# Kernel tuning notes

Measured on AMD Instinct MI355X. Metric: run time of the kernel, lower is better.

Reference implementation:

```python
import jax, jax.numpy as jnp
import numpy as np

TOPK = 10
STEP = 0.1

def setup_inputs() -> dict:
    key = jax.random.key(0)
    k1, k2 = jax.random.split(key)
    input = jax.random.normal(k1, (65536, 2048), dtype=jnp.float32)
    target = jax.random.normal(k2, (65536,), dtype=jnp.float32)
    return {"input": input, "target": target}

def reference(input, target):
    # topk over last dim: values [N,k], indices [N,k]
    values, indices = jax.lax.top_k(input, TOPK)
    # diag(value @ (index*step+1).T) == row-wise dot product
    weights = indices.astype(values.dtype) * STEP + 1.0
    pred = jnp.sum(values * weights, axis=-1)  # [N]
    return jnp.mean(jnp.square(target - pred))
```

## Files before the change

kernel.cpp:

```cpp
#include <hip/hip_runtime.h>

#define COLS 2048
#define TOPK 10

typedef float f32x4 __attribute__((ext_vector_type(4)));

__global__ __launch_bounds__(256, 4) void topk_mse_main(
    const float* __restrict__ input,
    const float* __restrict__ target,
    float* __restrict__ partials)
{
    const int lane = threadIdx.x & 63;
    const int wv   = threadIdx.x >> 6;
    const int row  = (blockIdx.x << 2) + wv;

    const f32x4* rp4 = reinterpret_cast<const f32x4*>(input + (size_t)row * COLS) + lane;
    const float tgt = target[row];

    float e[32];
#pragma unroll
    for (int j = 0; j < 8; ++j) {
        f32x4 v = __builtin_nontemporal_load(rp4 + j * 64);
        e[4*j+0] = v.x; e[4*j+1] = v.y; e[4*j+2] = v.z; e[4*j+3] = v.w;
    }

    float m16[16];
#pragma unroll
    for (int i = 0; i < 16; ++i) m16[i] = fmaxf(e[2*i], e[2*i+1]);
#pragma unroll
    for (int i = 0; i < 8; ++i)  m16[i] = fmaxf(m16[2*i], m16[2*i+1]);
#pragma unroll
    for (int i = 0; i < 4; ++i)  m16[i] = fmaxf(m16[2*i], m16[2*i+1]);
    float m0 = fmaxf(fmaxf(m16[0], m16[1]), fmaxf(m16[2], m16[3]));

    float s = m0;
#pragma unroll
    for (int k = 2; k <= 64; k <<= 1) {
        const bool bk = (lane & k) != 0;
#pragma unroll
        for (int j = k >> 1; j > 0; j >>= 1) {
            float p = __shfl_xor(s, j);
            const bool take_min = (((lane & j) != 0) == bk);
            s = take_min ? fminf(s, p) : fmaxf(s, p);
        }
    }
    const float t0 = __shfl(s, 64 - TOPK);

    const float A = 1.0f + 0.4f * (float)lane;
    float s0 = 0.0f, s1 = 0.0f, s2 = 0.0f, s3 = 0.0f;
    int cnt = 0;
#pragma unroll
    for (int i = 0; i < 32; ++i) {
        const bool c = (e[i] >= t0);
        cnt += __popcll(__ballot(c));
        const float m = c ? e[i] : 0.0f;
        const float offw = 0.1f * (float)(((i >> 2) << 8) + (i & 3));
        if ((i & 3) == 0)      { s0 = fmaf(m, A, fmaf(m, offw, s0)); }
        else if ((i & 3) == 1) { s1 = fmaf(m, A, fmaf(m, offw, s1)); }
        else if ((i & 3) == 2) { s2 = fmaf(m, A, fmaf(m, offw, s2)); }
        else                   { s3 = fmaf(m, A, fmaf(m, offw, s3)); }
    }
    float sum = (s0 + s1) + (s2 + s3);
#pragma unroll
    for (int off = 32; off >= 1; off >>= 1)
        sum += __shfl_xor(sum, off);

    int excess = cnt - TOPK;
    unsigned removed = 0;
    while (excess > 0) {
        float lv = __builtin_inff();
        int   lc = -1;
#pragma unroll
        for (int i = 0; i < 32; ++i) {
            const int col = (lane << 2) + ((i >> 2) << 8) + (i & 3);
            const bool act = (e[i] >= t0) && !((removed >> i) & 1u);
            const bool better = act && ((e[i] < lv) || (e[i] == lv && col > lc));
            lv = better ? e[i] : lv;
            lc = better ? col  : lc;
        }
#pragma unroll
        for (int off = 32; off >= 1; off >>= 1) {
            const float pv = __shfl_xor(lv, off);
            const int   pc = __shfl_xor(lc, off);
            const bool take = (pv < lv) || (pv == lv && pc > lc);
            lv = take ? pv : lv;
            lc = take ? pc : lc;
        }
        sum -= lv * ((float)lc * 0.1f + 1.0f);
        if (((lc >> 2) & 63) == lane) {
            const int i = ((lc >> 8) << 2) | (lc & 3);
            removed |= (1u << i);
        }
        --excess;
    }

    __shared__ float ps[4];
    if (lane == 0) {
        const float d = tgt - sum;
        ps[wv] = d * d;
    }
    __syncthreads();
    if (threadIdx.x == 0)
        partials[blockIdx.x] = (ps[0] + ps[1]) + (ps[2] + ps[3]);
}

__global__ __launch_bounds__(256) void topk_mse_reduce(
    const float* __restrict__ partials,
    float* __restrict__ out,
    int nb, float inv_n)
{
    const f32x4* p4 = reinterpret_cast<const f32x4*>(partials);
    const int nv = nb >> 2;
    double s = 0.0;
    for (int i = threadIdx.x; i < nv; i += 256) {
        f32x4 v = p4[i];
        s += (double)v.x + (double)v.y + (double)v.z + (double)v.w;
    }
#pragma unroll
    for (int off = 32; off >= 1; off >>= 1) s += __shfl_xor(s, off);
    __shared__ double ws[4];
    const int wv = threadIdx.x >> 6;
    if ((threadIdx.x & 63) == 0) ws[wv] = s;
    __syncthreads();
    if (threadIdx.x == 0)
        out[0] = (float)(((ws[0] + ws[1]) + (ws[2] + ws[3])) * (double)inv_n);
}

extern "C" void kernel_launch(void* const* d_in, const int* in_sizes, int n_in,
                              void* d_out, int out_size, void* d_ws, size_t ws_size,
                              hipStream_t stream) {
    const float* input  = (const float*)d_in[0];
    const float* target = (const float*)d_in[1];
    float* out = (float*)d_out;
    float* partials = (float*)d_ws;

    const int rows = in_sizes[1];
    const int nb = rows / 4;
    const float inv_n = 1.0f / (float)rows;

    topk_mse_main<<<nb, 256, 0, stream>>>(input, target, partials);
    topk_mse_reduce<<<1, 256, 0, stream>>>(partials, out, nb, inv_n);
}
```

Baseline: 90.83 us.

## Make waves persistent over 16 rows with double-buffered register row prefetch

The kernel now launches a fixed 4096 waves (1024 blocks), each processing 16 rows strided by 4096. The next row is loaded into a second register buffer while the current row's top-10 selection and weighted sum run, so memory latency overlaps with compute. Each wave accumulates its squared errors in double and writes one partial, which removes the per-block shared-memory reduction and shrinks the partials array. The cost is doubled register use per thread (64 floats of row data), which can lower occupancy, and the row count is hardcoded to 65536.

```diff
diff --git a/kernel.cpp b/kernel.cpp
--- a/kernel.cpp
+++ b/kernel.cpp
@@ -2,28 +2,23 @@
 
 #define COLS 2048
 #define TOPK 10
+#define NWAVES 4096
+#define RPW 16
 
 typedef float f32x4 __attribute__((ext_vector_type(4)));
 
-__global__ __launch_bounds__(256, 4) void topk_mse_main(
-    const float* __restrict__ input,
-    const float* __restrict__ target,
-    float* __restrict__ partials)
-{
-    const int lane = threadIdx.x & 63;
-    const int wv   = threadIdx.x >> 6;
-    const int row  = (blockIdx.x << 2) + wv;
-
+__device__ __forceinline__ void load_row(const float* __restrict__ input,
+                                         int row, int lane, float (&e)[32]) {
     const f32x4* rp4 = reinterpret_cast<const f32x4*>(input + (size_t)row * COLS) + lane;
-    const float tgt = target[row];
-
-    float e[32];
 #pragma unroll
     for (int j = 0; j < 8; ++j) {
         f32x4 v = __builtin_nontemporal_load(rp4 + j * 64);
         e[4*j+0] = v.x; e[4*j+1] = v.y; e[4*j+2] = v.z; e[4*j+3] = v.w;
     }
+}
 
+__device__ __forceinline__ float row_weighted_top10(const float (&e)[32],
+                                                    int lane, float A) {
     float m16[16];
 #pragma unroll
     for (int i = 0; i < 16; ++i) m16[i] = fmaxf(e[2*i], e[2*i+1]);
@@ -46,8 +41,7 @@
     }
     const float t0 = __shfl(s, 64 - TOPK);
 
-    const float A = 1.0f + 0.4f * (float)lane;
-    float s0 = 0.0f, s1 = 0.0f, s2 = 0.0f, s3 = 0.0f;
+    float s0 = 0.f, s1 = 0.f, s2 = 0.f, s3 = 0.f;
     int cnt = 0;
 #pragma unroll
     for (int i = 0; i < 32; ++i) {
@@ -55,15 +49,14 @@
         cnt += __popcll(__ballot(c));
         const float m = c ? e[i] : 0.0f;
         const float offw = 0.1f * (float)(((i >> 2) << 8) + (i & 3));
-        if ((i & 3) == 0)      { s0 = fmaf(m, A, fmaf(m, offw, s0)); }
-        else if ((i & 3) == 1) { s1 = fmaf(m, A, fmaf(m, offw, s1)); }
-        else if ((i & 3) == 2) { s2 = fmaf(m, A, fmaf(m, offw, s2)); }
-        else                   { s3 = fmaf(m, A, fmaf(m, offw, s3)); }
+        if ((i & 3) == 0)      s0 = fmaf(m, A, fmaf(m, offw, s0));
+        else if ((i & 3) == 1) s1 = fmaf(m, A, fmaf(m, offw, s1));
+        else if ((i & 3) == 2) s2 = fmaf(m, A, fmaf(m, offw, s2));
+        else                   s3 = fmaf(m, A, fmaf(m, offw, s3));
     }
     float sum = (s0 + s1) + (s2 + s3);
 #pragma unroll
-    for (int off = 32; off >= 1; off >>= 1)
-        sum += __shfl_xor(sum, off);
+    for (int off = 32; off >= 1; off >>= 1) sum += __shfl_xor(sum, off);
 
     int excess = cnt - TOPK;
     unsigned removed = 0;
@@ -87,35 +80,66 @@
             lc = take ? pc : lc;
         }
         sum -= lv * ((float)lc * 0.1f + 1.0f);
-        if (((lc >> 2) & 63) == lane) {
-            const int i = ((lc >> 8) << 2) | (lc & 3);
-            removed |= (1u << i);
-        }
+        if (((lc >> 2) & 63) == lane)
+            removed |= (1u << (((lc >> 8) << 2) | (lc & 3)));
         --excess;
     }
+    return sum;
+}
 
-    __shared__ float ps[4];
-    if (lane == 0) {
-        const float d = tgt - sum;
-        ps[wv] = d * d;
+__global__ __launch_bounds__(256, 4) void topk_mse_main(
+    const float* __restrict__ input,
+    const float* __restrict__ target,
+    double* __restrict__ partials)
+{
+    const int lane = threadIdx.x & 63;
+    const int wv   = threadIdx.x >> 6;
+    const int gw   = (blockIdx.x << 2) + wv;
+    const float A  = 1.0f + 0.4f * (float)lane;
+
+    float ea[32], eb[32];
+    double acc = 0.0;
+
+    int row = gw;
+    load_row(input, row, lane, ea);
+    float tga = target[row];
+
+#pragma unroll 1
+    for (int it = 0; it < RPW; it += 2) {
+        const int rb = row + NWAVES;
+        float tgb = 0.0f;
+        if (it + 1 < RPW) {
+            load_row(input, rb, lane, eb);
+            tgb = target[rb];
+        }
+        {
+            const float p = row_weighted_top10(ea, lane, A);
+            const float d = tga - p;
+            acc += (double)(d * d);
+        }
+        const int ra = row + 2 * NWAVES;
+        if (it + 2 < RPW) {
+            load_row(input, ra, lane, ea);
+            tga = target[ra];
+        }
+        if (it + 1 < RPW) {
+            const float p = row_weighted_top10(eb, lane, A);
+            const float d = tgb - p;
+            acc += (double)(d * d);
+        }
+        row = ra;
     }
-    __syncthreads();
-    if (threadIdx.x == 0)
-        partials[blockIdx.x] = (ps[0] + ps[1]) + (ps[2] + ps[3]);
+
+    if (lane == 0) partials[gw] = acc;
 }
 
 __global__ __launch_bounds__(256) void topk_mse_reduce(
-    const float* __restrict__ partials,
+    const double* __restrict__ partials,
     float* __restrict__ out,
-    int nb, float inv_n)
+    int n, float inv_n)
 {
-    const f32x4* p4 = reinterpret_cast<const f32x4*>(partials);
-    const int nv = nb >> 2;
     double s = 0.0;
-    for (int i = threadIdx.x; i < nv; i += 256) {
-        f32x4 v = p4[i];
-        s += (double)v.x + (double)v.y + (double)v.z + (double)v.w;
-    }
+    for (int i = threadIdx.x; i < n; i += 256) s += partials[i];
 #pragma unroll
     for (int off = 32; off >= 1; off >>= 1) s += __shfl_xor(s, off);
     __shared__ double ws[4];
@@ -132,12 +156,11 @@
     const float* input  = (const float*)d_in[0];
     const float* target = (const float*)d_in[1];
     float* out = (float*)d_out;
-    float* partials = (float*)d_ws;
+    double* partials = (double*)d_ws;
 
     const int rows = in_sizes[1];
-    const int nb = rows / 4;
     const float inv_n = 1.0f / (float)rows;
 
-    topk_mse_main<<<nb, 256, 0, stream>>>(input, target, partials);
-    topk_mse_reduce<<<1, 256, 0, stream>>>(partials, out, nb, inv_n);
+    topk_mse_main<<<NWAVES / 4, 256, 0, stream>>>(input, target, partials);
+    topk_mse_reduce<<<1, 256, 0, stream>>>(partials, out, NWAVES, inv_n);
 }
```

After: 115.9 us. +27.6%, slower.
